# Kernel optimization log

Hardware: AMD Instinct MI355X
Metric: run time of the kernel (lower is better)

## Reference

```python
import jax, jax.numpy as jnp
import numpy as np

B, S, D, H = 4, 2048, 1024, 16
HS = D // H          # head size 64
DF = 4 * D           # ffn hidden 4096
EPS = 1e-5


def _layer_norm(x, g, b):
    mu = jnp.mean(x, axis=-1, keepdims=True)
    var = jnp.var(x, axis=-1, keepdims=True)
    return (x - mu) * jax.lax.rsqrt(var + EPS) * g + b


def setup_inputs() -> dict:
    key = jax.random.key(0)
    ks = jax.random.split(key, 12)
    s_d = 1.0 / np.sqrt(D)
    s_f = 1.0 / np.sqrt(DF)
    return {
        "x": jax.random.normal(ks[0], (B, S, D), jnp.float32),
        # per-head q/k/v projections, batched over heads: [H, D, HS]
        "wq": jax.random.uniform(ks[1], (H, D, HS), jnp.float32, -s_d, s_d),
        "wk": jax.random.uniform(ks[2], (H, D, HS), jnp.float32, -s_d, s_d),
        "wv": jax.random.uniform(ks[3], (H, D, HS), jnp.float32, -s_d, s_d),
        "proj_w": jax.random.uniform(ks[4], (D, D), jnp.float32, -s_d, s_d),
        "proj_b": jax.random.uniform(ks[5], (D,), jnp.float32, -s_d, s_d),
        "ff1_w": jax.random.uniform(ks[6], (D, DF), jnp.float32, -s_d, s_d),
        "ff1_b": jax.random.uniform(ks[7], (DF,), jnp.float32, -s_d, s_d),
        "ff2_w": jax.random.uniform(ks[8], (DF, D), jnp.float32, -s_f, s_f),
        "ff2_b": jax.random.uniform(ks[9], (D,), jnp.float32, -s_f, s_f),
        "ln1_g": jnp.ones((D,), jnp.float32),
        "ln1_b": jnp.zeros((D,), jnp.float32),
        "ln2_g": jnp.ones((D,), jnp.float32),
        "ln2_b": jnp.zeros((D,), jnp.float32),
    }


def reference(x, wq, wk, wv, proj_w, proj_b, ff1_w, ff1_b, ff2_w, ff2_b,
              ln1_g, ln1_b, ln2_g, ln2_b):
    # --- multi-head causal self-attention on ln1(x), all heads batched ---
    h = _layer_norm(x, ln1_g, ln1_b)                      # [B,S,D]
    q = jnp.einsum("bsd,hde->bhse", h, wq)                # [B,H,S,HS]
    k = jnp.einsum("bsd,hde->bhse", h, wk)
    v = jnp.einsum("bsd,hde->bhse", h, wv)
    scale = HS ** -0.5
    scores = jnp.einsum("bhse,bhte->bhst", q, k) * scale  # [B,H,S,S]
    causal = jnp.tril(jnp.ones((S, S), bool))
    scores = jnp.where(causal, scores, jnp.finfo(scores.dtype).min)
    att = jax.nn.softmax(scores, axis=-1)
    o = jnp.einsum("bhst,bhte->bhse", att, v)             # [B,H,S,HS]
    o = o.transpose(0, 2, 1, 3).reshape(B, S, D)          # concat heads
    sa = o @ proj_w + proj_b
    x = x + sa
    # --- FFN on ln2(x) ---
    h2 = _layer_norm(x, ln2_g, ln2_b)
    ff = jax.nn.relu(h2 @ ff1_w + ff1_b) @ ff2_w + ff2_b
    return x + ff
```

## Files before the change

kernel.cpp:

```cpp
#include <hip/hip_runtime.h>
#include <hip/hip_bf16.h>

#define BB 4
#define SS 2048
#define DD 1024
#define HH 16
#define HSZ 64
#define DFF 4096

typedef short short8 __attribute__((ext_vector_type(8)));
typedef float f32x4 __attribute__((ext_vector_type(4)));
typedef unsigned short us4 __attribute__((ext_vector_type(4)));

#define AS1 __attribute__((address_space(1)))
#define AS3 __attribute__((address_space(3)))

__device__ __forceinline__ unsigned short f2bf(float f) {
    return __bfloat16_as_ushort(__float2bfloat16(f));
}

__global__ __launch_bounds__(256) void pack_qkv_kernel(
    const float* __restrict__ wq, const float* __restrict__ wk,
    const float* __restrict__ wv, __hip_bfloat16* __restrict__ out)
{
    int id = blockIdx.x * 256 + threadIdx.x;
    int n = id >> 10;
    int k = id & 1023;
    int sel = n >> 10;
    int hn = n & 1023;
    int h = hn >> 6, e = hn & 63;
    const float* src = (sel == 0) ? wq : (sel == 1) ? wk : wv;
    out[id] = __float2bfloat16(src[(size_t)h * (DD * HSZ) + (size_t)k * HSZ + e]);
}

__global__ __launch_bounds__(256) void pack_T_kernel(
    const float* __restrict__ in, __hip_bfloat16* __restrict__ out, int K, int N)
{
    int id = blockIdx.x * 256 + threadIdx.x;
    int n = id / K;
    int k = id - n * K;
    out[id] = __float2bfloat16(in[(size_t)k * N + n]);
}

__global__ __launch_bounds__(256) void ln_kernel(
    const float* __restrict__ x, const float* __restrict__ g,
    const float* __restrict__ b, __hip_bfloat16* __restrict__ out)
{
    int row = blockIdx.x;
    int t = threadIdx.x;
    const float4* xr = (const float4*)(x + (size_t)row * DD);
    float4 v = xr[t];
    float s = v.x + v.y + v.z + v.w;
    float ss = v.x * v.x + v.y * v.y + v.z * v.z + v.w * v.w;
    #pragma unroll
    for (int off = 32; off; off >>= 1) {
        s += __shfl_xor(s, off, 64);
        ss += __shfl_xor(ss, off, 64);
    }
    __shared__ float red[8];
    int w = t >> 6, lane = t & 63;
    if (lane == 0) { red[w] = s; red[4 + w] = ss; }
    __syncthreads();
    s = red[0] + red[1] + red[2] + red[3];
    ss = red[4] + red[5] + red[6] + red[7];
    float mu = s * (1.f / DD);
    float var = ss * (1.f / DD) - mu * mu;
    float rs = rsqrtf(var + 1e-5f);
    float4 gv = ((const float4*)g)[t];
    float4 bv = ((const float4*)b)[t];
    ushort4 pk = make_ushort4(
        f2bf((v.x - mu) * rs * gv.x + bv.x),
        f2bf((v.y - mu) * rs * gv.y + bv.y),
        f2bf((v.z - mu) * rs * gv.z + bv.z),
        f2bf((v.w - mu) * rs * gv.w + bv.w));
    *(ushort4*)((unsigned short*)out + (size_t)row * DD + t * 4) = pk;
}

template<bool BIAS, bool RELU, bool RES, bool OUTF32>
__global__ __launch_bounds__(256) void gemm_kernel(
    const __hip_bfloat16* __restrict__ A, const __hip_bfloat16* __restrict__ BT,
    const float* __restrict__ bias, const float* __restrict__ res,
    void* __restrict__ Cout, int M, int N, int K, int nbx)
{
    __shared__ uint4 As[512];
    __shared__ uint4 Bs[512];
    const int t = threadIdx.x;
    const int lane = t & 63, w = t >> 6;
    const int nwg = gridDim.x;
    const int cpx = nwg >> 3;
    const int wg = blockIdx.x;
    const int swz = (wg & 7) * cpx + (wg >> 3);
    const int bx = swz % nbx, by = swz / nbx;
    const int row0 = by * 128, col0 = bx * 128;
    const int wr = (w >> 1) * 64, wc = (w & 1) * 64;
    const int lr = lane & 15, kb = lane >> 4;
    f32x4 acc[4][4] = {};

    for (int k0 = 0; k0 < K; k0 += 32) {
        __syncthreads();
        #pragma unroll
        for (int j = 0; j < 2; ++j) {
            int s = w * 128 + j * 64 + lane;
            int r = s >> 2;
            int fkb = (s & 3) ^ ((r >> 1) & 3);
            const __hip_bfloat16* asrc = A + (size_t)(row0 + r) * K + k0 + fkb * 8;
            const __hip_bfloat16* bsrc = BT + (size_t)(col0 + r) * K + k0 + fkb * 8;
            __builtin_amdgcn_global_load_lds((const AS1 void*)asrc, (AS3 void*)&As[w * 128 + j * 64], 16, 0, 0);
            __builtin_amdgcn_global_load_lds((const AS1 void*)bsrc, (AS3 void*)&Bs[w * 128 + j * 64], 16, 0, 0);
        }
        __syncthreads();
        short8 af[4], bfr[4];
        #pragma unroll
        for (int m = 0; m < 4; ++m) {
            int r = wr + m * 16 + lr;
            af[m] = *(const short8*)&As[r * 4 + (kb ^ ((r >> 1) & 3))];
        }
        #pragma unroll
        for (int n = 0; n < 4; ++n) {
            int c = wc + n * 16 + lr;
            bfr[n] = *(const short8*)&Bs[c * 4 + (kb ^ ((c >> 1) & 3))];
        }
        #pragma unroll
        for (int m = 0; m < 4; ++m)
            #pragma unroll
            for (int n = 0; n < 4; ++n)
                acc[m][n] = __builtin_amdgcn_mfma_f32_16x16x32_bf16(af[m], bfr[n], acc[m][n], 0, 0, 0);
    }

    #pragma unroll
    for (int m = 0; m < 4; ++m) {
        #pragma unroll
        for (int j = 0; j < 4; ++j) {
            int rr = row0 + wr + m * 16 + (lane >> 4) * 4 + j;
            #pragma unroll
            for (int n = 0; n < 4; ++n) {
                int cc = col0 + wc + n * 16 + lr;
                float vv = acc[m][n][j];
                if (BIAS) vv += bias[cc];
                if (RELU) vv = fmaxf(vv, 0.f);
                if (RES) vv += res[(size_t)rr * N + cc];
                if (OUTF32) ((float*)Cout)[(size_t)rr * N + cc] = vv;
                else ((__hip_bfloat16*)Cout)[(size_t)rr * N + cc] = __float2bfloat16(vv);
            }
        }
    }
}

__device__ __forceinline__ void stage_kv(
    const unsigned short* __restrict__ qkvu, size_t rowbase, int h, int kv0, int tl,
    unsigned short* __restrict__ Kb, unsigned short* __restrict__ Vb)
{
    {
        int kv = tl >> 2, c = tl & 3;
        const unsigned short* src = qkvu + rowbase + (size_t)(kv0 + kv) * 3072 + DD + h * HSZ + c * 16;
        uint4 v0 = *(const uint4*)src;
        uint4 v1 = *(const uint4*)(src + 8);
        int sw = kv & 7;
        *(uint4*)&Kb[kv * 64 + ((2 * c) ^ sw) * 8] = v0;
        *(uint4*)&Kb[kv * 64 + ((2 * c + 1) ^ sw) * 8] = v1;
    }
    {
        int bkv = ((tl >> 6) << 2) | (tl & 3);
        int bd = (tl >> 2) & 15;
        const unsigned short* src = qkvu + rowbase + (size_t)(kv0 + bkv * 4) * 3072 + 2 * DD + h * HSZ + bd * 4;
        us4 r0 = *(const us4*)src;
        us4 r1 = *(const us4*)(src + 3072);
        us4 r2 = *(const us4*)(src + 2 * 3072);
        us4 r3 = *(const us4*)(src + 3 * 3072);
        #pragma unroll
        for (int cc = 0; cc < 4; ++cc) {
            int d = bd * 4 + cc;
            us4 wv = { r0[cc], r1[cc], r2[cc], r3[cc] };
            *(us4*)&Vb[d * 64 + (((bkv >> 1) ^ (d & 7)) * 8) + (bkv & 1) * 4] = wv;
        }
    }
}

__device__ __forceinline__ void flash_tile(
    const unsigned short* __restrict__ Kb, const unsigned short* __restrict__ Vb,
    unsigned short* __restrict__ Pw, const short8* qfc, int qgc, int kv0, int q, int g,
    float& m_run, float& l_run, f32x4* oacc)
{
    f32x4 st[4] = {};
    __builtin_amdgcn_s_setprio(1);
    #pragma unroll
    for (int tt = 0; tt < 4; ++tt) {
        #pragma unroll
        for (int kk = 0; kk < 2; ++kk) {
            short8 kf = *(const short8*)&Kb[(tt * 16 + q) * 64 + ((4 * kk + g) ^ (q & 7)) * 8];
            st[tt] = __builtin_amdgcn_mfma_f32_16x16x32_bf16(kf, qfc[kk], st[tt], 0, 0, 0);
        }
    }
    __builtin_amdgcn_s_setprio(0);

    float mt = -1e30f;
    #pragma unroll
    for (int tt = 0; tt < 4; ++tt)
        #pragma unroll
        for (int j = 0; j < 4; ++j) {
            float s = st[tt][j] * 0.125f;
            int kvg = kv0 + tt * 16 + g * 4 + j;
            s = (kvg <= qgc) ? s : -1e30f;
            st[tt][j] = s;
            mt = fmaxf(mt, s);
        }
    mt = fmaxf(mt, __shfl_xor(mt, 16, 64));
    mt = fmaxf(mt, __shfl_xor(mt, 32, 64));
    float m_new = fmaxf(m_run, mt);
    float corr = __expf(m_run - m_new);
    float lsum = 0.f;
    #pragma unroll
    for (int tt = 0; tt < 4; ++tt)
        #pragma unroll
        for (int j = 0; j < 4; ++j) {
            float p = __expf(st[tt][j] - m_new);
            st[tt][j] = p;
            lsum += p;
        }
    lsum += __shfl_xor(lsum, 16, 64);
    lsum += __shfl_xor(lsum, 32, 64);
    l_run = l_run * corr + lsum;
    m_run = m_new;

    #pragma unroll
    for (int tt = 0; tt < 4; ++tt) {
        unsigned int lo = ((unsigned int)f2bf(st[tt][1]) << 16) | (unsigned int)f2bf(st[tt][0]);
        unsigned int hi = ((unsigned int)f2bf(st[tt][3]) << 16) | (unsigned int)f2bf(st[tt][2]);
        uint2 pk = make_uint2(lo, hi);
        *(uint2*)&Pw[q * 64 + ((2 * tt + (g >> 1)) ^ (q & 7)) * 8 + (g & 1) * 4] = pk;
    }

    #pragma unroll
    for (int j = 0; j < 4; ++j) {
        float cj = __shfl(corr, g * 4 + j, 64);
        #pragma unroll
        for (int dn = 0; dn < 4; ++dn)
            oacc[dn][j] *= cj;
    }

    __builtin_amdgcn_s_setprio(1);
    #pragma unroll
    for (int kk = 0; kk < 2; ++kk) {
        short8 pf = *(const short8*)&Pw[q * 64 + ((4 * kk + g) ^ (q & 7)) * 8];
        #pragma unroll
        for (int dn = 0; dn < 4; ++dn) {
            short8 vf = *(const short8*)&Vb[(dn * 16 + q) * 64 + ((4 * kk + g) ^ (q & 7)) * 8];
            oacc[dn] = __builtin_amdgcn_mfma_f32_16x16x32_bf16(pf, vf, oacc[dn], 0, 0, 0);
        }
    }
    __builtin_amdgcn_s_setprio(0);
}

__global__ __launch_bounds__(512) void attn_kernel(
    const __hip_bfloat16* __restrict__ qkv, __hip_bfloat16* __restrict__ o)
{
    __shared__ unsigned short K_lds[2][64 * 64];
    __shared__ unsigned short Vt_lds[2][64 * 64];
    __shared__ unsigned short P_lds[8 * 1024];

    const int t = threadIdx.x;
    const int lane = t & 63, w = t >> 6;
    const int grp = w >> 2, wq4 = w & 3, tl = t & 255;
    const int q = lane & 15, g = lane >> 4;
    const int pq = blockIdx.x & 15;
    const int h = (blockIdx.x >> 4) & 15;
    const int b = blockIdx.x >> 8;
    const int qtA = pq, qtB = 31 - pq;
    const int qt1 = grp ? qtB : qtA;
    const unsigned short* qkvu = (const unsigned short*)qkv;
    const size_t rowbase = (size_t)(b * SS) * 3072;
    unsigned short* Kb = K_lds[grp];
    unsigned short* Vb = Vt_lds[grp];
    unsigned short* Pw = &P_lds[w * 1024];
    unsigned short* op = (unsigned short*)o;

    int qgc = qt1 * 64 + wq4 * 16 + q;
    short8 qfc[2];
    #pragma unroll
    for (int kk = 0; kk < 2; ++kk)
        qfc[kk] = *(const short8*)(qkvu + rowbase + (size_t)qgc * 3072 + h * HSZ + kk * 32 + g * 8);

    f32x4 oacc[4] = {};
    float m_run = -1e30f, l_run = 0.f;

    for (int it = 0; it <= pq; ++it) {
        __syncthreads();
        stage_kv(qkvu, rowbase, h, it * 64, tl, Kb, Vb);
        __syncthreads();
        flash_tile(Kb, Vb, Pw, qfc, qgc, it * 64, q, g, m_run, l_run, oacc);
    }

    if (grp == 0) {
        #pragma unroll
        for (int j = 0; j < 4; ++j) {
            float lj = __shfl(l_run, g * 4 + j, 64);
            float inv = 1.f / lj;
            int orow = qtA * 64 + wq4 * 16 + g * 4 + j;
            #pragma unroll
            for (int dn = 0; dn < 4; ++dn)
                op[(size_t)(b * SS + orow) * DD + h * HSZ + dn * 16 + q] = f2bf(oacc[dn][j] * inv);
        }
        qgc = qtB * 64 + wq4 * 16 + q;
        #pragma unroll
        for (int kk = 0; kk < 2; ++kk)
            qfc[kk] = *(const short8*)(qkvu + rowbase + (size_t)qgc * 3072 + h * HSZ + kk * 32 + g * 8);
        m_run = -1e30f; l_run = 0.f;
        #pragma unroll
        for (int dn = 0; dn < 4; ++dn) oacc[dn] = f32x4{0.f, 0.f, 0.f, 0.f};
    }

    for (int it2 = 0; it2 < 16 - pq; ++it2) {
        int tile = grp ? (pq + 1 + it2) : (16 + it2);
        bool active = grp ? (tile <= 15) : true;
        __syncthreads();
        if (active) stage_kv(qkvu, rowbase, h, tile * 64, tl, Kb, Vb);
        __syncthreads();
        if (active) flash_tile(Kb, Vb, Pw, qfc, qgc, tile * 64, q, g, m_run, l_run, oacc);
    }

    __syncthreads();
    float* obuf = (float*)K_lds;
    float* mlbuf = (float*)P_lds;
    if (grp == 0) {
        #pragma unroll
        for (int dn = 0; dn < 4; ++dn)
            #pragma unroll
            for (int j = 0; j < 4; ++j)
                obuf[wq4 * 1024 + lane * 16 + dn * 4 + j] = oacc[dn][j];
        if (g == 0) { mlbuf[wq4 * 32 + q] = m_run; mlbuf[wq4 * 32 + 16 + q] = l_run; }
    }
    __syncthreads();
    if (grp == 1) {
        float mA = mlbuf[wq4 * 32 + q];
        float lA = mlbuf[wq4 * 32 + 16 + q];
        float mM = fmaxf(m_run, mA);
        float sB = __expf(m_run - mM);
        float sA = __expf(mA - mM);
        float lM = l_run * sB + lA * sA;
        #pragma unroll
        for (int j = 0; j < 4; ++j) {
            float sBj = __shfl(sB, g * 4 + j, 64);
            float sAj = __shfl(sA, g * 4 + j, 64);
            float lMj = __shfl(lM, g * 4 + j, 64);
            float inv = 1.f / lMj;
            int orow = qtB * 64 + wq4 * 16 + g * 4 + j;
            #pragma unroll
            for (int dn = 0; dn < 4; ++dn) {
                float oA = obuf[wq4 * 1024 + lane * 16 + dn * 4 + j];
                float vv = (oacc[dn][j] * sBj + oA * sAj) * inv;
                op[(size_t)(b * SS + orow) * DD + h * HSZ + dn * 16 + q] = f2bf(vv);
            }
        }
    }
}

extern "C" void kernel_launch(void* const* d_in, const int* in_sizes, int n_in,
                              void* d_out, int out_size, void* d_ws, size_t ws_size,
                              hipStream_t stream)
{
    const float* x      = (const float*)d_in[0];
    const float* wq     = (const float*)d_in[1];
    const float* wk     = (const float*)d_in[2];
    const float* wv     = (const float*)d_in[3];
    const float* proj_w = (const float*)d_in[4];
    const float* proj_b = (const float*)d_in[5];
    const float* ff1_w  = (const float*)d_in[6];
    const float* ff1_b  = (const float*)d_in[7];
    const float* ff2_w  = (const float*)d_in[8];
    const float* ff2_b  = (const float*)d_in[9];
    const float* ln1_g  = (const float*)d_in[10];
    const float* ln1_b  = (const float*)d_in[11];
    const float* ln2_g  = (const float*)d_in[12];
    const float* ln2_b  = (const float*)d_in[13];
    float* out = (float*)d_out;

    char* ws = (char*)d_ws;
    const size_t MB = 1ull << 20;
    __hip_bfloat16* h     = (__hip_bfloat16*)(ws);
    __hip_bfloat16* qkv   = (__hip_bfloat16*)(ws + 16 * MB);
    __hip_bfloat16* obuf  = (__hip_bfloat16*)(ws + 64 * MB);
    float*          x1    = (float*)(ws + 80 * MB);
    __hip_bfloat16* wqkvT = (__hip_bfloat16*)(ws + 112 * MB);
    __hip_bfloat16* projT = (__hip_bfloat16*)(ws + 118 * MB);
    __hip_bfloat16* ff1T  = (__hip_bfloat16*)(ws + 120 * MB);
    __hip_bfloat16* ff2T  = (__hip_bfloat16*)(ws + 128 * MB);
    __hip_bfloat16* f1    = (__hip_bfloat16*)(ws + 16 * MB);

    const int ROWS = BB * SS;

    pack_qkv_kernel<<<(3 * DD * DD) / 256, 256, 0, stream>>>(wq, wk, wv, wqkvT);
    pack_T_kernel<<<(DD * DD) / 256, 256, 0, stream>>>(proj_w, projT, DD, DD);
    pack_T_kernel<<<(DD * DFF) / 256, 256, 0, stream>>>(ff1_w, ff1T, DD, DFF);
    pack_T_kernel<<<(DFF * DD) / 256, 256, 0, stream>>>(ff2_w, ff2T, DFF, DD);

    ln_kernel<<<ROWS, 256, 0, stream>>>(x, ln1_g, ln1_b, h);
    gemm_kernel<false, false, false, false><<<(3 * DD / 128) * (ROWS / 128), 256, 0, stream>>>(
        h, wqkvT, nullptr, nullptr, qkv, ROWS, 3 * DD, DD, 3 * DD / 128);
    attn_kernel<<<BB * HH * 16, 512, 0, stream>>>(qkv, obuf);
    gemm_kernel<true, false, true, true><<<(DD / 128) * (ROWS / 128), 256, 0, stream>>>(
        obuf, projT, proj_b, x, x1, ROWS, DD, DD, DD / 128);
    ln_kernel<<<ROWS, 256, 0, stream>>>(x1, ln2_g, ln2_b, h);
    gemm_kernel<true, true, false, false><<<(DFF / 128) * (ROWS / 128), 256, 0, stream>>>(
        h, ff1T, ff1_b, nullptr, f1, ROWS, DFF, DD, DFF / 128);
    gemm_kernel<true, false, true, true><<<(DD / 128) * (ROWS / 128), 256, 0, stream>>>(
        f1, ff2T, ff2_b, x1, out, ROWS, DD, DFF, DD / 128);
}
```

Measured before the change: 486.1 us.

## Double-buffer GEMM with larger 256-row tiles, BK=64 and 512 threads

Rewrites the bf16 GEMM to use 256xBN tiles (BN=256 for QKV/FF1, 128 for proj/FF2) with 8 waves and a K-step of 64. LDS is double-buffered, and the next tile is issued with global_load_lds before computing the current one, using vmcnt waits instead of full syncs. MFMA sections are raised with setprio. The goal is to hide global-load latency and raise arithmetic intensity per tile. In exchange, LDS use and accumulator registers rise, which may lower occupancy, and the fixed vmcnt counts depend on how many loads the compiler emits.

```diff
diff --git a/kernel.cpp b/kernel.cpp
--- a/kernel.cpp
+++ b/kernel.cpp
@@ -76,66 +76,110 @@
     *(ushort4*)((unsigned short*)out + (size_t)row * DD + t * 4) = pk;
 }
 
-template<bool BIAS, bool RELU, bool RES, bool OUTF32>
-__global__ __launch_bounds__(256) void gemm_kernel(
+template<int BN, bool BIAS, bool RELU, bool RES, bool OUTF32>
+__global__ __launch_bounds__(512) void gemm_kernel(
     const __hip_bfloat16* __restrict__ A, const __hip_bfloat16* __restrict__ BT,
     const float* __restrict__ bias, const float* __restrict__ res,
     void* __restrict__ Cout, int M, int N, int K, int nbx)
 {
-    __shared__ uint4 As[512];
-    __shared__ uint4 Bs[512];
+    constexpr int WN = (BN == 256) ? 4 : 2;
+    constexpr int MREP = (BN == 256) ? 8 : 4;
+    constexpr int BLOADS = BN / 64;
+    __shared__ uint4 As[2][2048];
+    __shared__ uint4 Bs[2][BN * 8];
+
     const int t = threadIdx.x;
     const int lane = t & 63, w = t >> 6;
+    const int lr = lane & 15, g = lane >> 4;
     const int nwg = gridDim.x;
     const int cpx = nwg >> 3;
     const int wg = blockIdx.x;
     const int swz = (wg & 7) * cpx + (wg >> 3);
     const int bx = swz % nbx, by = swz / nbx;
-    const int row0 = by * 128, col0 = bx * 128;
-    const int wr = (w >> 1) * 64, wc = (w & 1) * 64;
-    const int lr = lane & 15, kb = lane >> 4;
-    f32x4 acc[4][4] = {};
-
-    for (int k0 = 0; k0 < K; k0 += 32) {
-        __syncthreads();
-        #pragma unroll
-        for (int j = 0; j < 2; ++j) {
-            int s = w * 128 + j * 64 + lane;
-            int r = s >> 2;
-            int fkb = (s & 3) ^ ((r >> 1) & 3);
-            const __hip_bfloat16* asrc = A + (size_t)(row0 + r) * K + k0 + fkb * 8;
-            const __hip_bfloat16* bsrc = BT + (size_t)(col0 + r) * K + k0 + fkb * 8;
-            __builtin_amdgcn_global_load_lds((const AS1 void*)asrc, (AS3 void*)&As[w * 128 + j * 64], 16, 0, 0);
-            __builtin_amdgcn_global_load_lds((const AS1 void*)bsrc, (AS3 void*)&Bs[w * 128 + j * 64], 16, 0, 0);
-        }
-        __syncthreads();
-        short8 af[4], bfr[4];
-        #pragma unroll
-        for (int m = 0; m < 4; ++m) {
-            int r = wr + m * 16 + lr;
-            af[m] = *(const short8*)&As[r * 4 + (kb ^ ((r >> 1) & 3))];
-        }
+    const int row0 = by * 256, col0 = bx * BN;
+    const int wr = (w / WN) * (MREP * 16), wc = (w % WN) * 64;
+
+    f32x4 acc[MREP][4] = {};
+    const int NT = K >> 6;
+
+    auto stage = [&](int buf, int k0) {
+        #pragma unroll
+        for (int j = 0; j < 4; ++j) {
+            int s = j * 512 + t;
+            int r = s >> 3;
+            int kb = (s & 7) ^ (r & 7);
+            const __hip_bfloat16* src = A + (size_t)(row0 + r) * K + k0 + kb * 8;
+            __builtin_amdgcn_global_load_lds((const AS1 void*)src,
+                (AS3 void*)(&As[buf][j * 512 + (t & ~63)]), 16, 0, 0);
+        }
+        #pragma unroll
+        for (int j = 0; j < BLOADS; ++j) {
+            int s = j * 512 + t;
+            int r = s >> 3;
+            int kb = (s & 7) ^ (r & 7);
+            const __hip_bfloat16* src = BT + (size_t)(col0 + r) * K + k0 + kb * 8;
+            __builtin_amdgcn_global_load_lds((const AS1 void*)src,
+                (AS3 void*)(&Bs[buf][j * 512 + (t & ~63)]), 16, 0, 0);
+        }
+    };
+
+    auto compute = [&](int buf) {
+        short8 bf[4][2];
         #pragma unroll
         for (int n = 0; n < 4; ++n) {
             int c = wc + n * 16 + lr;
-            bfr[n] = *(const short8*)&Bs[c * 4 + (kb ^ ((c >> 1) & 3))];
-        }
-        #pragma unroll
-        for (int m = 0; m < 4; ++m)
-            #pragma unroll
-            for (int n = 0; n < 4; ++n)
-                acc[m][n] = __builtin_amdgcn_mfma_f32_16x16x32_bf16(af[m], bfr[n], acc[m][n], 0, 0, 0);
-    }
-
-    #pragma unroll
-    for (int m = 0; m < 4; ++m) {
-        #pragma unroll
-        for (int j = 0; j < 4; ++j) {
-            int rr = row0 + wr + m * 16 + (lane >> 4) * 4 + j;
+            #pragma unroll
+            for (int kk = 0; kk < 2; ++kk)
+                bf[n][kk] = *(const short8*)&Bs[buf][c * 8 + ((kk * 4 + g) ^ (c & 7))];
+        }
+        #pragma unroll
+        for (int ph = 0; ph < MREP / 2; ++ph) {
+            short8 af[2][2];
+            #pragma unroll
+            for (int m2 = 0; m2 < 2; ++m2) {
+                int r = wr + ph * 32 + m2 * 16 + lr;
+                #pragma unroll
+                for (int kk = 0; kk < 2; ++kk)
+                    af[m2][kk] = *(const short8*)&As[buf][r * 8 + ((kk * 4 + g) ^ (r & 7))];
+            }
+            __builtin_amdgcn_s_setprio(1);
+            #pragma unroll
+            for (int m2 = 0; m2 < 2; ++m2)
+                #pragma unroll
+                for (int n = 0; n < 4; ++n)
+                    #pragma unroll
+                    for (int kk = 0; kk < 2; ++kk)
+                        acc[ph * 2 + m2][n] = __builtin_amdgcn_mfma_f32_16x16x32_bf16(
+                            af[m2][kk], bf[n][kk], acc[ph * 2 + m2][n], 0, 0, 0);
+            __builtin_amdgcn_s_setprio(0);
+        }
+    };
+
+    stage(0, 0);
+    int cur = 0;
+    for (int tt = 0; tt < NT - 1; ++tt) {
+        stage(cur ^ 1, (tt + 1) * 64);
+        if constexpr (BN == 256) asm volatile("s_waitcnt vmcnt(8)" ::: "memory");
+        else                     asm volatile("s_waitcnt vmcnt(6)" ::: "memory");
+        __builtin_amdgcn_s_barrier();
+        compute(cur);
+        __builtin_amdgcn_sched_barrier(0);
+        __builtin_amdgcn_s_barrier();
+        cur ^= 1;
+    }
+    asm volatile("s_waitcnt vmcnt(0)" ::: "memory");
+    __builtin_amdgcn_s_barrier();
+    compute(cur);
+
+    #pragma unroll
+    for (int mi = 0; mi < MREP; ++mi) {
+        #pragma unroll
+        for (int j = 0; j < 4; ++j) {
+            int rr = row0 + wr + mi * 16 + g * 4 + j;
             #pragma unroll
             for (int n = 0; n < 4; ++n) {
                 int cc = col0 + wc + n * 16 + lr;
-                float vv = acc[m][n][j];
+                float vv = acc[mi][n][j];
                 if (BIAS) vv += bias[cc];
                 if (RELU) vv = fmaxf(vv, 0.f);
                 if (RES) vv += res[(size_t)rr * N + cc];
@@ -394,14 +438,14 @@
     pack_T_kernel<<<(DFF * DD) / 256, 256, 0, stream>>>(ff2_w, ff2T, DFF, DD);
 
     ln_kernel<<<ROWS, 256, 0, stream>>>(x, ln1_g, ln1_b, h);
-    gemm_kernel<false, false, false, false><<<(3 * DD / 128) * (ROWS / 128), 256, 0, stream>>>(
-        h, wqkvT, nullptr, nullptr, qkv, ROWS, 3 * DD, DD, 3 * DD / 128);
+    gemm_kernel<256, false, false, false, false><<<(ROWS / 256) * (3 * DD / 256), 512, 0, stream>>>(
+        h, wqkvT, nullptr, nullptr, qkv, ROWS, 3 * DD, DD, 3 * DD / 256);
     attn_kernel<<<BB * HH * 16, 512, 0, stream>>>(qkv, obuf);
-    gemm_kernel<true, false, true, true><<<(DD / 128) * (ROWS / 128), 256, 0, stream>>>(
+    gemm_kernel<128, true, false, true, true><<<(ROWS / 256) * (DD / 128), 512, 0, stream>>>(
         obuf, projT, proj_b, x, x1, ROWS, DD, DD, DD / 128);
     ln_kernel<<<ROWS, 256, 0, stream>>>(x1, ln2_g, ln2_b, h);
-    gemm_kernel<true, true, false, false><<<(DFF / 128) * (ROWS / 128), 256, 0, stream>>>(
-        h, ff1T, ff1_b, nullptr, f1, ROWS, DFF, DD, DFF / 128);
-    gemm_kernel<true, false, true, true><<<(DD / 128) * (ROWS / 128), 256, 0, stream>>>(
+    gemm_kernel<256, true, true, false, false><<<(ROWS / 256) * (DFF / 256), 512, 0, stream>>>(
+        h, ff1T, ff1_b, nullptr, f1, ROWS, DFF, DD, DFF / 256);
+    gemm_kernel<128, true, false, true, true><<<(ROWS / 256) * (DD / 128), 512, 0, stream>>>(
         f1, ff2T, ff2_b, x1, out, ROWS, DD, DFF, DD / 128);
 }
```

Result: faster. 441.9 us (-9.1%).
